# Performance work log

Measured on AMD Instinct MI355X. Metric: run time of the kernel, lower is better.

The kernel has to match this reference:

```python
import jax, jax.numpy as jnp
import numpy as np

TEMPERATURE = 0.07
TIME_THRESH = 5.0 * 1e6  # microseconds


def setup_inputs() -> dict:
    key = jax.random.key(0)
    k1, k2, k3 = jax.random.split(key, 3)
    B, D = 8192, 512
    desc = jax.random.normal(k1, (B, D), dtype=jnp.float32)
    desc = desc / jnp.linalg.norm(desc, axis=-1, keepdims=True)  # module expects normalized descriptors
    seq_ids = jax.random.randint(k2, (B,), 0, 64, dtype=jnp.int64)
    time_mid = jax.random.randint(k3, (B,), 0, 20_000_000, dtype=jnp.int64)
    return {"descriptors": desc, "seq_ids": seq_ids, "time_mid": time_mid}


def reference(descriptors, seq_ids, time_mid):
    B = descriptors.shape[0]
    # [B, B] temperature-scaled cosine similarities
    logits = jnp.matmul(descriptors, descriptors.T) / TEMPERATURE

    eye = jnp.eye(B, dtype=bool)
    same_seq = seq_ids[:, None] == seq_ids[None, :]
    close_time = jnp.abs(time_mid[:, None] - time_mid[None, :]).astype(jnp.float32) < TIME_THRESH
    pos_mask = same_seq & close_time & ~eye  # positives
    offdiag = ~eye                            # positives + negatives = denominator support

    # denominator per row i: log sum_{j != i} exp(logits[i, j])
    denom_lse = jax.nn.logsumexp(jnp.where(offdiag, logits, -jnp.inf), axis=1)  # [B]

    # per positive pair (i, j): -log( exp(l_ij) / denom_i ) = denom_lse_i - l_ij
    pair_loss = jnp.where(pos_mask, denom_lse[:, None] - logits, 0.0)
    num_pos = jnp.sum(pos_mask)
    loss = jnp.sum(pair_loss) / jnp.maximum(num_pos, 1).astype(pair_loss.dtype)
    return loss
```

## Files before the change

kernel.cpp:

```cpp
#include <hip/hip_runtime.h>
#include <math.h>

#define TILE 128

typedef __attribute__((ext_vector_type(4))) float f32x4;
typedef __attribute__((ext_vector_type(2))) long long llong2;

#define INV_T    14.285714285714286f
#define K2C      20.60992915f
#define K2C8     0.32203014296875f
#define INV_T64  0.22321428571428573f
#define TIME_THR 5000000

__device__ __forceinline__ unsigned pack_bf16x2(float lo, float hi) {
  unsigned a = __float_as_uint(lo);
  unsigned b = __float_as_uint(hi);
  a = (a + 0x7FFFu + ((a >> 16) & 1u)) >> 16;
  b = (b + 0x7FFFu + ((b >> 16) & 1u)) & 0xFFFF0000u;
  return b | a;
}

__device__ __forceinline__ unsigned f32_to_e4m3(float x) {
  unsigned u = __float_as_uint(x);
  unsigned s = (u >> 24) & 0x80u;
  int e = (int)((u >> 23) & 0xffu) - 127;
  unsigned m = u & 0x7fffffu;
  if (e < -9) return s;
  if (e < -6) {
    int sh = 20 + (-6 - e);
    unsigned full = (1u << 23) | m;
    unsigned q = full >> sh;
    unsigned rem = full & ((1u << sh) - 1u);
    unsigned half = 1u << (sh - 1);
    if (rem > half || (rem == half && (q & 1u))) q++;
    return s | q;
  }
  unsigned q = m >> 20;
  unsigned rem = m & 0xfffffu;
  if (rem > 0x80000u || (rem == 0x80000u && (q & 1u))) q++;
  int ee = e;
  if (q == 8u) { q = 0u; ee++; }
  if (ee > 8 || (ee == 8 && q == 7u)) return s | 0x7eu;
  return s | (unsigned)((ee + 7) << 3) | q;
}

__device__ __forceinline__ void gl_lds16(const void* g, void* l) {
  __builtin_amdgcn_global_load_lds(
      (const __attribute__((address_space(1))) unsigned int*)g,
      (__attribute__((address_space(3))) unsigned int*)l, 16, 0, 0);
}

template <int MODE>
__device__ __forceinline__ void infonce_body(
    const float* __restrict__ desc, const unsigned char* __restrict__ desc8,
    const int* __restrict__ seq, const int* __restrict__ tmid,
    float* __restrict__ p_se, float* __restrict__ p_ps,
    float* __restrict__ p_pc, int B, int D, int NB) {
  const int T = NB * (NB + 1) / 2;
  int t = blockIdx.x;
  if ((T & 7) == 0) t = (t & 7) * (T >> 3) + (t >> 3);
  float fn = (float)NB + 0.5f;
  int r = (int)(fn - sqrtf(fmaxf(fn * fn - 2.0f * (float)t, 0.0f)));
  if (r < 0) r = 0;
  if (r > NB - 1) r = NB - 1;
  auto Sf = [NB](int rr) { return rr * NB - ((rr * (rr - 1)) >> 1); };
  while (r > 0 && Sf(r) > t) --r;
  while (r < NB - 1 && Sf(r + 1) <= t) ++r;
  const int rb = r;
  const int cb = rb + (t - Sf(rb));
  const bool upper = (cb != rb);

  const int row0 = rb * TILE;
  const int col0 = cb * TILE;

  const int tid = threadIdx.x;
  const int l = tid & 63;
  const int w = tid >> 6;
  const int wrow = (w >> 1) << 6;
  const int wcol = (w & 1) << 6;
  const int lr = l & 15;
  const int kg = l >> 4;

  f32x4 acc[4][4];
#pragma unroll
  for (int m = 0; m < 4; ++m)
#pragma unroll
    for (int n = 0; n < 4; ++n) acc[m][n] = (f32x4){0.f, 0.f, 0.f, 0.f};

  const int sr = tid >> 3;
  const int sc = tid & 7;

  if (MODE == 2) {
    __shared__ __align__(16) unsigned char lA8[2][TILE][128];
    __shared__ __align__(16) unsigned char lB8[TILE][128];
    __shared__ int mseq_r[TILE], mtim_r[TILE], mseq_c[TILE], mtim_c[TILE];

    if (tid < TILE) {
      mseq_r[tid] = seq[row0 + tid];
      mtim_r[tid] = tmid[row0 + tid];
      mseq_c[tid] = seq[col0 + tid];
      mtim_c[tid] = tmid[col0 + tid];
    }

    const int NT = D >> 7;
    const unsigned char* pa =
        desc8 + (size_t)(row0 + (tid >> 3)) * D + (tid & 7) * 16;
    const unsigned char* pb =
        desc8 + (size_t)(col0 + (tid >> 3)) * D + (tid & 7) * 16;
    const size_t rstep = (size_t)32 * D;

    auto stageA = [&](int bu_, int tt) {
      const int off = tt << 7;
#pragma unroll
      for (int q = 0; q < 4; ++q)
        gl_lds16(pa + (size_t)q * rstep + off,
                 (char*)&lA8[bu_][0][0] + (q << 12) + tid * 16);
    };
    auto stageB = [&](int tt) {
      const int off = tt << 7;
#pragma unroll
      for (int q = 0; q < 4; ++q)
        gl_lds16(pb + (size_t)q * rstep + off,
                 (char*)&lB8[0][0] + (q << 12) + tid * 16);
    };

    __builtin_amdgcn_sched_barrier(0);
    stageA(0, 0);
    stageB(0);
    __builtin_amdgcn_sched_barrier(0);

    for (int ts = 0; ts < NT; ++ts) {
      const int bu = ts & 1;
      if (ts + 1 < NT) {
        stageA(bu ^ 1, ts + 1);
        __builtin_amdgcn_sched_barrier(0);
        asm volatile("s_waitcnt vmcnt(4)" ::: "memory");
      } else {
        asm volatile("s_waitcnt vmcnt(0)" ::: "memory");
      }
      __builtin_amdgcn_sched_barrier(0);
      __builtin_amdgcn_s_barrier();
      __builtin_amdgcn_sched_barrier(0);

      llong2 av[4][2], bv[4][2];
#pragma unroll
      for (int m = 0; m < 4; ++m) {
        const int row = wrow + (m << 4) + lr;
#pragma unroll
        for (int j2 = 0; j2 < 2; ++j2) {
          const int ch = ((j2 << 2) + kg) ^ (row & 7);
          av[m][j2] =
              *reinterpret_cast<const llong2*>(&lA8[bu][row][ch << 4]);
        }
      }
#pragma unroll
      for (int n = 0; n < 4; ++n) {
        const int row = wcol + (n << 4) + lr;
#pragma unroll
        for (int j2 = 0; j2 < 2; ++j2) {
          const int ch = ((j2 << 2) + kg) ^ (row & 7);
          bv[n][j2] = *reinterpret_cast<const llong2*>(&lB8[row][ch << 4]);
        }
      }
      __builtin_amdgcn_sched_barrier(0);
      asm volatile("s_waitcnt lgkmcnt(0)" ::: "memory");
      __builtin_amdgcn_sched_barrier(0);
      __builtin_amdgcn_s_setprio(1);
#pragma unroll
      for (int j2 = 0; j2 < 2; ++j2)
#pragma unroll
        for (int kk = 0; kk < 2; ++kk)
#pragma unroll
          for (int m = 0; m < 4; ++m)
#pragma unroll
            for (int n = 0; n < 4; ++n)
              acc[m][n] = __builtin_amdgcn_mfma_f32_16x16x32_fp8_fp8(
                  av[m][j2][kk], bv[n][j2][kk], acc[m][n], 0, 0, 0);
      __builtin_amdgcn_s_setprio(0);
      __builtin_amdgcn_sched_barrier(0);
      __builtin_amdgcn_s_barrier();
      __builtin_amdgcn_sched_barrier(0);
      if (ts + 1 < NT) stageB(ts + 1);
      __builtin_amdgcn_sched_barrier(0);
    }
    __syncthreads();

    float* rowred = (float*)&lA8[0][0][0];
    float* colred = (float*)&lB8[0][0];

    int cseq[4], ctim[4], gcol[4];
#pragma unroll
    for (int n = 0; n < 4; ++n) {
      const int cl = wcol + (n << 4) + lr;
      cseq[n] = mseq_c[cl];
      ctim[n] = mtim_c[cl];
      gcol[n] = col0 + cl;
    }
    float colse[4] = {0.f, 0.f, 0.f, 0.f};
    float colpd[4] = {0.f, 0.f, 0.f, 0.f};
    float colpc[4] = {0.f, 0.f, 0.f, 0.f};

#pragma unroll
    for (int m = 0; m < 4; ++m) {
#pragma unroll
      for (int reg = 0; reg < 4; ++reg) {
        const int rl = wrow + (m << 4) + (kg << 2) + reg;
        const int growg = row0 + rl;
        const int rs = mseq_r[rl];
        const int rt = mtim_r[rl];
        float se = 0.f, pd = 0.f, pcnt = 0.f;
#pragma unroll
        for (int n = 0; n < 4; ++n) {
          const float dot = acc[m][n][reg];
          const float e = exp2f(fmaf(dot, K2C8, -K2C));
          const bool nd = (growg != gcol[n]);
          int dt = rt - ctim[n];
          dt = dt < 0 ? -dt : dt;
          const bool pos = nd && (rs == cseq[n]) && (dt < TIME_THR);
          const float ev = nd ? e : 0.f;
          const float dv = pos ? dot : 0.f;
          const float cv = pos ? 1.f : 0.f;
          se += ev;
          pd += dv;
          pcnt += cv;
          colse[n] += ev;
          colpd[n] += dv;
          colpc[n] += cv;
        }
#pragma unroll
        for (int s = 1; s < 16; s <<= 1) {
          se += __shfl_xor(se, s);
          pd += __shfl_xor(pd, s);
          pcnt += __shfl_xor(pcnt, s);
        }
        if (lr == 0) {
          const int half = wcol >> 6;
          float* rr3 = rowred + ((size_t)(half * TILE + rl)) * 3;
          rr3[0] = se;
          rr3[1] = pd;
          rr3[2] = pcnt;
        }
      }
    }
    if (upper) {
#pragma unroll
      for (int n = 0; n < 4; ++n) {
        float cs = colse[n], cp = colpd[n], cc = colpc[n];
        cs += __shfl_xor(cs, 16);
        cp += __shfl_xor(cp, 16);
        cc += __shfl_xor(cc, 16);
        cs += __shfl_xor(cs, 32);
        cp += __shfl_xor(cp, 32);
        cc += __shfl_xor(cc, 32);
        if (l < 16) {
          const int half = wrow >> 6;
          const int cl = wcol + (n << 4) + lr;
          float* cr3 = colred + ((size_t)(half * TILE + cl)) * 3;
          cr3[0] = cs;
          cr3[1] = cp;
          cr3[2] = cc;
        }
      }
    }
    __syncthreads();

    if (tid < TILE) {
      const int row = tid;
      const float se =
          rowred[(size_t)row * 3 + 0] + rowred[(size_t)(TILE + row) * 3 + 0];
      const float pd =
          rowred[(size_t)row * 3 + 1] + rowred[(size_t)(TILE + row) * 3 + 1];
      const float pc =
          rowred[(size_t)row * 3 + 2] + rowred[(size_t)(TILE + row) * 3 + 2];
      const size_t o = (size_t)cb * B + row0 + row;
      p_se[o] = se;
      p_ps[o] = pd * INV_T64;
      p_pc[o] = pc;
    } else if (upper && tid < 2 * TILE) {
      const int col = tid - TILE;
      const float se =
          colred[(size_t)col * 3 + 0] + colred[(size_t)(TILE + col) * 3 + 0];
      const float pd =
          colred[(size_t)col * 3 + 1] + colred[(size_t)(TILE + col) * 3 + 1];
      const float pc =
          colred[(size_t)col * 3 + 2] + colred[(size_t)(TILE + col) * 3 + 2];
      const size_t o = (size_t)rb * B + col0 + col;
      p_se[o] = se;
      p_ps[o] = pd * INV_T64;
      p_pc[o] = pc;
    }
  } else {
    __shared__ __align__(16) unsigned short lAw[TILE][64];
    __shared__ __align__(16) unsigned short lBw[TILE][64];
    __shared__ int mseq_r[TILE], mtim_r[TILE], mseq_c[TILE], mtim_c[TILE];
    typedef __attribute__((ext_vector_type(8))) short short8v;

    if (tid < TILE) {
      mseq_r[tid] = seq[row0 + tid];
      mtim_r[tid] = tmid[row0 + tid];
      mseq_c[tid] = seq[col0 + tid];
      mtim_c[tid] = tmid[col0 + tid];
    }
    for (int k0 = 0; k0 < D; k0 += 64) {
      __syncthreads();
#pragma unroll
      for (int p = 0; p < 4; ++p) {
        const int rr = (p << 5) + sr;
        const float* gA = desc + (size_t)(row0 + rr) * D + k0 + (sc << 3);
        const float4 fa0 = *reinterpret_cast<const float4*>(gA);
        const float4 fa1 = *reinterpret_cast<const float4*>(gA + 4);
        const float* gB = desc + (size_t)(col0 + rr) * D + k0 + (sc << 3);
        const float4 fb0 = *reinterpret_cast<const float4*>(gB);
        const float4 fb1 = *reinterpret_cast<const float4*>(gB + 4);
        uint4 wa, wb;
        wa.x = pack_bf16x2(fa0.x, fa0.y);
        wa.y = pack_bf16x2(fa0.z, fa0.w);
        wa.z = pack_bf16x2(fa1.x, fa1.y);
        wa.w = pack_bf16x2(fa1.z, fa1.w);
        wb.x = pack_bf16x2(fb0.x, fb0.y);
        wb.y = pack_bf16x2(fb0.z, fb0.w);
        wb.z = pack_bf16x2(fb1.x, fb1.y);
        wb.w = pack_bf16x2(fb1.z, fb1.w);
        const int dst = (sc ^ (rr & 7)) << 3;
        *reinterpret_cast<uint4*>(&lAw[rr][dst]) = wa;
        *reinterpret_cast<uint4*>(&lBw[rr][dst]) = wb;
      }
      __syncthreads();
#pragma unroll
      for (int kk = 0; kk < 2; ++kk) {
        short8v af[4], bf[4];
#pragma unroll
        for (int m = 0; m < 4; ++m) {
          const int rowa = wrow + (m << 4) + lr;
          const int ch = ((kk << 2) + kg) ^ (rowa & 7);
          af[m] = *reinterpret_cast<const short8v*>(&lAw[rowa][ch << 3]);
        }
#pragma unroll
        for (int n = 0; n < 4; ++n) {
          const int rowb = wcol + (n << 4) + lr;
          const int ch = ((kk << 2) + kg) ^ (rowb & 7);
          bf[n] = *reinterpret_cast<const short8v*>(&lBw[rowb][ch << 3]);
        }
#pragma unroll
        for (int m = 0; m < 4; ++m)
#pragma unroll
          for (int n = 0; n < 4; ++n)
            acc[m][n] = __builtin_amdgcn_mfma_f32_16x16x32_bf16(af[m], bf[n],
                                                                acc[m][n], 0, 0, 0);
      }
    }
    __syncthreads();

    int cseq[4], ctim[4], gcol[4];
#pragma unroll
    for (int n = 0; n < 4; ++n) {
      const int cl = wcol + (n << 4) + lr;
      cseq[n] = mseq_c[cl];
      ctim[n] = mtim_c[cl];
      gcol[n] = col0 + cl;
    }
    float colse[4] = {0.f, 0.f, 0.f, 0.f};
    float colpd[4] = {0.f, 0.f, 0.f, 0.f};
    float colpc[4] = {0.f, 0.f, 0.f, 0.f};

#pragma unroll
    for (int m = 0; m < 4; ++m) {
#pragma unroll
      for (int reg = 0; reg < 4; ++reg) {
        const int rl = wrow + (m << 4) + (kg << 2) + reg;
        const int growg = row0 + rl;
        const int rs = mseq_r[rl];
        const int rt = mtim_r[rl];
        float se = 0.f, pd = 0.f, pcnt = 0.f;
#pragma unroll
        for (int n = 0; n < 4; ++n) {
          const float dot = acc[m][n][reg];
          const float e = exp2f(fmaf(dot, K2C, -K2C));
          const bool nd = (growg != gcol[n]);
          int dt = rt - ctim[n];
          dt = dt < 0 ? -dt : dt;
          const bool pos = nd && (rs == cseq[n]) && (dt < TIME_THR);
          const float ev = nd ? e : 0.f;
          const float dv = pos ? dot : 0.f;
          const float cv = pos ? 1.f : 0.f;
          se += ev;
          pd += dv;
          pcnt += cv;
          if (upper) {
            colse[n] += ev;
            colpd[n] += dv;
            colpc[n] += cv;
          }
        }
#pragma unroll
        for (int s = 1; s < 16; s <<= 1) {
          se += __shfl_xor(se, s);
          pd += __shfl_xor(pd, s);
          pcnt += __shfl_xor(pcnt, s);
        }
        if ((l & 15) == 0) {
          atomicAdd(&p_se[growg], se);
          atomicAdd(&p_ps[growg], pd * INV_T);
          atomicAdd(&p_pc[growg], pcnt);
        }
      }
    }
    if (upper) {
#pragma unroll
      for (int n = 0; n < 4; ++n) {
        float cs = colse[n], cp = colpd[n], cc = colpc[n];
        cs += __shfl_xor(cs, 16);
        cp += __shfl_xor(cp, 16);
        cc += __shfl_xor(cc, 16);
        cs += __shfl_xor(cs, 32);
        cp += __shfl_xor(cp, 32);
        cc += __shfl_xor(cc, 32);
        if (kg == 0) {
          atomicAdd(&p_se[gcol[n]], cs);
          atomicAdd(&p_ps[gcol[n]], cp * INV_T);
          atomicAdd(&p_pc[gcol[n]], cc);
        }
      }
    }
  }
}

__global__ __launch_bounds__(256, 3) void infonce_main2(
    const float* desc, const unsigned char* desc8, const int* seq,
    const int* tmid, float* p_se, float* p_ps, float* p_pc, int B, int D,
    int NB) {
  infonce_body<2>(desc, desc8, seq, tmid, p_se, p_ps, p_pc, B, D, NB);
}
__global__ __launch_bounds__(256, 2) void infonce_main0(
    const float* desc, const unsigned char* desc8, const int* seq,
    const int* tmid, float* p_se, float* p_ps, float* p_pc, int B, int D,
    int NB) {
  infonce_body<0>(desc, desc8, seq, tmid, p_se, p_ps, p_pc, B, D, NB);
}

__global__ __launch_bounds__(256) void conv_fp8(const float* __restrict__ in,
                                                unsigned char* __restrict__ out,
                                                int D, int nchunk) {
  const int u = blockIdx.x * 256 + threadIdx.x;
  if (u >= nchunk) return;
  const int cpr = D >> 4;
  const int r = u / cpr;
  const int cc = u - r * cpr;
  const int kt = cc >> 3;
  const int p = cc & 7;
  const int g = p ^ (r & 7);
  const int j2 = g >> 2;
  const int kgc = g & 3;
  const float* src = in + (size_t)r * D + (kt << 7) + (j2 << 6) + (kgc << 3);
  const float4 f0 = *reinterpret_cast<const float4*>(src);
  const float4 f1 = *reinterpret_cast<const float4*>(src + 4);
  const float4 g0 = *reinterpret_cast<const float4*>(src + 32);
  const float4 g1 = *reinterpret_cast<const float4*>(src + 36);
  unsigned char b[16];
  b[0] = f32_to_e4m3(f0.x * 8.f);
  b[1] = f32_to_e4m3(f0.y * 8.f);
  b[2] = f32_to_e4m3(f0.z * 8.f);
  b[3] = f32_to_e4m3(f0.w * 8.f);
  b[4] = f32_to_e4m3(f1.x * 8.f);
  b[5] = f32_to_e4m3(f1.y * 8.f);
  b[6] = f32_to_e4m3(f1.z * 8.f);
  b[7] = f32_to_e4m3(f1.w * 8.f);
  b[8] = f32_to_e4m3(g0.x * 8.f);
  b[9] = f32_to_e4m3(g0.y * 8.f);
  b[10] = f32_to_e4m3(g0.z * 8.f);
  b[11] = f32_to_e4m3(g0.w * 8.f);
  b[12] = f32_to_e4m3(g1.x * 8.f);
  b[13] = f32_to_e4m3(g1.y * 8.f);
  b[14] = f32_to_e4m3(g1.z * 8.f);
  b[15] = f32_to_e4m3(g1.w * 8.f);
  uint4 wv;
  unsigned* wp = (unsigned*)&wv;
#pragma unroll
  for (int d = 0; d < 4; ++d)
    wp[d] = (unsigned)b[d * 4] | ((unsigned)b[d * 4 + 1] << 8) |
            ((unsigned)b[d * 4 + 2] << 16) | ((unsigned)b[d * 4 + 3] << 24);
  *reinterpret_cast<uint4*>(out + (size_t)u * 16) = wv;
}

__global__ __launch_bounds__(256) void reduce_parts4(
    const float* __restrict__ p_se, const float* __restrict__ p_ps,
    const float* __restrict__ p_pc, float* __restrict__ bnum,
    float* __restrict__ bcnt, int B, int NB) {
  const int tid = threadIdx.x;
  const int rloc = tid & 63;
  const int chunk = tid >> 6;
  const int row = blockIdx.x * 64 + rloc;
  const int jpc = NB >> 2;
  float se = 0.f, ps = 0.f, pc = 0.f;
  for (int j = chunk * jpc; j < (chunk + 1) * jpc; ++j) {
    const size_t o = (size_t)j * B + row;
    se += p_se[o];
    ps += p_ps[o];
    pc += p_pc[o];
  }
  __shared__ float s3[3][4][64];
  s3[0][chunk][rloc] = se;
  s3[1][chunk][rloc] = ps;
  s3[2][chunk][rloc] = pc;
  __syncthreads();
  if (tid < 64) {
    const float tse = s3[0][0][tid] + s3[0][1][tid] + s3[0][2][tid] + s3[0][3][tid];
    const float tps = s3[1][0][tid] + s3[1][1][tid] + s3[1][2][tid] + s3[1][3][tid];
    const float tpc = s3[2][0][tid] + s3[2][1][tid] + s3[2][2][tid] + s3[2][3][tid];
    float a = tpc * (logf(tse) + INV_T) - tps;
    float b = tpc;
#pragma unroll
    for (int s = 1; s < 64; s <<= 1) {
      a += __shfl_xor(a, s);
      b += __shfl_xor(b, s);
    }
    if (tid == 0) {
      bnum[blockIdx.x] = a;
      bcnt[blockIdx.x] = b;
    }
  }
}

__global__ __launch_bounds__(256) void final_reduce(
    const float* __restrict__ bnum, const float* __restrict__ bcnt,
    float* __restrict__ out, int n) {
  __shared__ float sn[256];
  __shared__ float sc[256];
  const int tid = threadIdx.x;
  float a = 0.f, b = 0.f;
  for (int i = tid; i < n; i += 256) {
    a += bnum[i];
    b += bcnt[i];
  }
  sn[tid] = a;
  sc[tid] = b;
  __syncthreads();
  for (int s = 128; s > 0; s >>= 1) {
    if (tid < s) {
      sn[tid] += sn[tid + s];
      sc[tid] += sc[tid + s];
    }
    __syncthreads();
  }
  if (tid == 0) out[0] = sn[0] / fmaxf(sc[0], 1.f);
}

__global__ __launch_bounds__(1024) void infonce_finalize(
    const float* __restrict__ a_se, const float* __restrict__ a_ps,
    const float* __restrict__ a_pc, float* __restrict__ out, int B) {
  __shared__ float sn[1024];
  __shared__ float sc[1024];
  const int tid = threadIdx.x;
  float num = 0.f, cnt = 0.f;
  for (int i = tid; i < B; i += 1024) {
    const float c = a_pc[i];
    num += c * (logf(a_se[i]) + INV_T) - a_ps[i];
    cnt += c;
  }
  sn[tid] = num;
  sc[tid] = cnt;
  __syncthreads();
  for (int s = 512; s > 0; s >>= 1) {
    if (tid < s) {
      sn[tid] += sn[tid + s];
      sc[tid] += sc[tid + s];
    }
    __syncthreads();
  }
  if (tid == 0) out[0] = sn[0] / fmaxf(sc[0], 1.f);
}

extern "C" void kernel_launch(void* const* d_in, const int* in_sizes, int n_in,
                              void* d_out, int out_size, void* d_ws, size_t ws_size,
                              hipStream_t stream) {
  (void)n_in;
  (void)out_size;
  const float* desc = (const float*)d_in[0];
  const int* seq = (const int*)d_in[1];
  const int* tmid = (const int*)d_in[2];
  const int B = in_sizes[1];
  const int D = in_sizes[0] / B;
  const int NB = B / TILE;
  const int T = NB * (NB + 1) / 2;

  const size_t desc8_bytes = (size_t)B * D;
  const size_t parts_elems = (size_t)B * NB;
  const size_t nb1 = (size_t)B / 64;
  const size_t need8 = desc8_bytes + 3 * parts_elems * 4 + 2 * nb1 * 4;

  if ((B & 255) == 0 && (D & 127) == 0 && ws_size >= need8) {
    unsigned char* desc8 = (unsigned char*)d_ws;
    float* p_se = (float*)((char*)d_ws + desc8_bytes);
    float* p_ps = p_se + parts_elems;
    float* p_pc = p_ps + parts_elems;
    float* bnum = p_pc + parts_elems;
    float* bcnt = bnum + nb1;
    const int nchunk = (int)(((size_t)B * D) >> 4);
    conv_fp8<<<(nchunk + 255) / 256, 256, 0, stream>>>(desc, desc8, D, nchunk);
    infonce_main2<<<T, 256, 0, stream>>>(desc, desc8, seq, tmid, p_se, p_ps,
                                         p_pc, B, D, NB);
    const int nrb = B / 64;
    reduce_parts4<<<nrb, 256, 0, stream>>>(p_se, p_ps, p_pc, bnum, bcnt, B, NB);
    final_reduce<<<1, 256, 0, stream>>>(bnum, bcnt, (float*)d_out, nrb);
  } else {
    float* a_se = (float*)d_ws;
    float* a_ps = a_se + B;
    float* a_pc = a_ps + B;
    hipMemsetAsync(d_ws, 0, (size_t)3 * B * sizeof(float), stream);
    infonce_main0<<<T, 256, 0, stream>>>(desc, nullptr, seq, tmid, a_se, a_ps,
                                         a_pc, B, D, NB);
    infonce_finalize<<<1, 1024, 0, stream>>>(a_se, a_ps, a_pc, (float*)d_out, B);
  }
}
```

Measured before the change: 109.7 us.

## Make FP8 tile kernel persistent and prefetch next tile across tile boundaries

Replaces the one-block-per-tile FP8 similarity kernel with a persistent kernel of up to 512 blocks that loop over triangular tiles. The first K-slice of the next tile is prefetched during the last K-step of the current one, so global-to-LDS loads overlap the epilogue. B is now double-buffered like A, and seq/time metadata is read from global memory instead of being staged in LDS. The larger LDS footprint at two blocks per CU lowers occupancy compared with the earlier three-blocks-per-CU launch bound, and the epilogue now issues global loads.

```diff
diff --git a/kernel.cpp b/kernel.cpp
--- a/kernel.cpp
+++ b/kernel.cpp
@@ -50,29 +50,17 @@
       (__attribute__((address_space(3))) unsigned int*)l, 16, 0, 0);
 }
 
-template <int MODE>
-__device__ __forceinline__ void infonce_body(
-    const float* __restrict__ desc, const unsigned char* __restrict__ desc8,
-    const int* __restrict__ seq, const int* __restrict__ tmid,
-    float* __restrict__ p_se, float* __restrict__ p_ps,
-    float* __restrict__ p_pc, int B, int D, int NB) {
+__global__ __launch_bounds__(256, 2) void infonce_pers(
+    const unsigned char* __restrict__ desc8, const int* __restrict__ seq,
+    const int* __restrict__ tmid, float* __restrict__ p_se,
+    float* __restrict__ p_ps, float* __restrict__ p_pc, int B, int D, int NB,
+    int G) {
+  __shared__ __align__(16) unsigned char lA8[2][TILE][128];
+  __shared__ __align__(16) unsigned char lB8[2][TILE][128];
+  __shared__ float redR[2 * TILE * 3];
+  __shared__ float redC[2 * TILE * 3];
+
   const int T = NB * (NB + 1) / 2;
-  int t = blockIdx.x;
-  if ((T & 7) == 0) t = (t & 7) * (T >> 3) + (t >> 3);
-  float fn = (float)NB + 0.5f;
-  int r = (int)(fn - sqrtf(fmaxf(fn * fn - 2.0f * (float)t, 0.0f)));
-  if (r < 0) r = 0;
-  if (r > NB - 1) r = NB - 1;
-  auto Sf = [NB](int rr) { return rr * NB - ((rr * (rr - 1)) >> 1); };
-  while (r > 0 && Sf(r) > t) --r;
-  while (r < NB - 1 && Sf(r + 1) <= t) ++r;
-  const int rb = r;
-  const int cb = rb + (t - Sf(rb));
-  const bool upper = (cb != rb);
-
-  const int row0 = rb * TILE;
-  const int col0 = cb * TILE;
-
   const int tid = threadIdx.x;
   const int l = tid & 63;
   const int w = tid >> 6;
@@ -80,6 +68,34 @@
   const int wcol = (w & 1) << 6;
   const int lr = l & 15;
   const int kg = l >> 4;
+  const int NT = D >> 7;
+
+  auto decode = [&](int idx, int& rb_, int& cb_) {
+    int t = idx;
+    if ((T & 7) == 0) t = (t & 7) * (T >> 3) + (t >> 3);
+    float fn = (float)NB + 0.5f;
+    int r = (int)(fn - sqrtf(fmaxf(fn * fn - 2.0f * (float)t, 0.0f)));
+    if (r < 0) r = 0;
+    if (r > NB - 1) r = NB - 1;
+    auto Sf = [&](int rr) { return rr * NB - ((rr * (rr - 1)) >> 1); };
+    while (r > 0 && Sf(r) > t) --r;
+    while (r < NB - 1 && Sf(r + 1) <= t) ++r;
+    rb_ = r;
+    cb_ = r + (t - Sf(r));
+  };
+
+  const size_t rstep = (size_t)32 * D;
+  const size_t lane_off = (size_t)(tid >> 3) * D + (size_t)(tid & 7) * 16;
+  auto stage = [&](const unsigned char* src, unsigned char* dst) {
+#pragma unroll
+    for (int q = 0; q < 4; ++q)
+      gl_lds16(src + (size_t)q * rstep, dst + (q << 12) + tid * 16);
+  };
+
+  int rb, cb;
+  decode(blockIdx.x, rb, cb);
+  const unsigned char* paCur = desc8 + (size_t)(rb * TILE) * D + lane_off;
+  const unsigned char* pbCur = desc8 + (size_t)(cb * TILE) * D + lane_off;
 
   f32x4 acc[4][4];
 #pragma unroll
@@ -87,54 +103,37 @@
 #pragma unroll
     for (int n = 0; n < 4; ++n) acc[m][n] = (f32x4){0.f, 0.f, 0.f, 0.f};
 
-  const int sr = tid >> 3;
-  const int sc = tid & 7;
-
-  if (MODE == 2) {
-    __shared__ __align__(16) unsigned char lA8[2][TILE][128];
-    __shared__ __align__(16) unsigned char lB8[TILE][128];
-    __shared__ int mseq_r[TILE], mtim_r[TILE], mseq_c[TILE], mtim_c[TILE];
-
-    if (tid < TILE) {
-      mseq_r[tid] = seq[row0 + tid];
-      mtim_r[tid] = tmid[row0 + tid];
-      mseq_c[tid] = seq[col0 + tid];
-      mtim_c[tid] = tmid[col0 + tid];
-    }
-
-    const int NT = D >> 7;
-    const unsigned char* pa =
-        desc8 + (size_t)(row0 + (tid >> 3)) * D + (tid & 7) * 16;
-    const unsigned char* pb =
-        desc8 + (size_t)(col0 + (tid >> 3)) * D + (tid & 7) * 16;
-    const size_t rstep = (size_t)32 * D;
-
-    auto stageA = [&](int bu_, int tt) {
-      const int off = tt << 7;
-#pragma unroll
-      for (int q = 0; q < 4; ++q)
-        gl_lds16(pa + (size_t)q * rstep + off,
-                 (char*)&lA8[bu_][0][0] + (q << 12) + tid * 16);
-    };
-    auto stageB = [&](int tt) {
-      const int off = tt << 7;
-#pragma unroll
-      for (int q = 0; q < 4; ++q)
-        gl_lds16(pb + (size_t)q * rstep + off,
-                 (char*)&lB8[0][0] + (q << 12) + tid * 16);
-    };
-
-    __builtin_amdgcn_sched_barrier(0);
-    stageA(0, 0);
-    stageB(0);
-    __builtin_amdgcn_sched_barrier(0);
+  __builtin_amdgcn_sched_barrier(0);
+  stage(paCur, &lA8[0][0][0]);
+  stage(pbCur, &lB8[0][0][0]);
+  __builtin_amdgcn_sched_barrier(0);
+
+  int gs = 0;
+  for (int j = blockIdx.x; j < T; j += G) {
+    const int row0 = rb * TILE;
+    const int col0 = cb * TILE;
+    const bool upper = (cb != rb);
+    const bool hasNext = (j + G < T);
+    int nrb = 0, ncb = 0;
+    const unsigned char *paNext = nullptr, *pbNext = nullptr;
+    if (hasNext) {
+      decode(j + G, nrb, ncb);
+      paNext = desc8 + (size_t)(nrb * TILE) * D + lane_off;
+      pbNext = desc8 + (size_t)(ncb * TILE) * D + lane_off;
+    }
 
     for (int ts = 0; ts < NT; ++ts) {
-      const int bu = ts & 1;
+      const int bu = gs & 1;
       if (ts + 1 < NT) {
-        stageA(bu ^ 1, ts + 1);
+        stage(paCur + ((ts + 1) << 7), &lA8[bu ^ 1][0][0]);
+        stage(pbCur + ((ts + 1) << 7), &lB8[bu ^ 1][0][0]);
         __builtin_amdgcn_sched_barrier(0);
-        asm volatile("s_waitcnt vmcnt(4)" ::: "memory");
+        asm volatile("s_waitcnt vmcnt(8)" ::: "memory");
+      } else if (hasNext) {
+        stage(paNext, &lA8[bu ^ 1][0][0]);
+        stage(pbNext, &lB8[bu ^ 1][0][0]);
+        __builtin_amdgcn_sched_barrier(0);
+        asm volatile("s_waitcnt vmcnt(8)" ::: "memory");
       } else {
         asm volatile("s_waitcnt vmcnt(0)" ::: "memory");
       }
@@ -159,7 +158,8 @@
 #pragma unroll
         for (int j2 = 0; j2 < 2; ++j2) {
           const int ch = ((j2 << 2) + kg) ^ (row & 7);
-          bv[n][j2] = *reinterpret_cast<const llong2*>(&lB8[row][ch << 4]);
+          bv[n][j2] =
+              *reinterpret_cast<const llong2*>(&lB8[bu][row][ch << 4]);
         }
       }
       __builtin_amdgcn_sched_barrier(0);
@@ -179,22 +179,16 @@
       __builtin_amdgcn_s_setprio(0);
       __builtin_amdgcn_sched_barrier(0);
       __builtin_amdgcn_s_barrier();
-      __builtin_amdgcn_sched_barrier(0);
-      if (ts + 1 < NT) stageB(ts + 1);
-      __builtin_amdgcn_sched_barrier(0);
-    }
-    __syncthreads();
-
-    float* rowred = (float*)&lA8[0][0][0];
-    float* colred = (float*)&lB8[0][0];
+      ++gs;
+    }
 
     int cseq[4], ctim[4], gcol[4];
 #pragma unroll
     for (int n = 0; n < 4; ++n) {
       const int cl = wcol + (n << 4) + lr;
-      cseq[n] = mseq_c[cl];
-      ctim[n] = mtim_c[cl];
       gcol[n] = col0 + cl;
+      cseq[n] = seq[gcol[n]];
+      ctim[n] = tmid[gcol[n]];
     }
     float colse[4] = {0.f, 0.f, 0.f, 0.f};
     float colpd[4] = {0.f, 0.f, 0.f, 0.f};
@@ -206,8 +200,8 @@
       for (int reg = 0; reg < 4; ++reg) {
         const int rl = wrow + (m << 4) + (kg << 2) + reg;
         const int growg = row0 + rl;
-        const int rs = mseq_r[rl];
-        const int rt = mtim_r[rl];
+        const int rs = seq[growg];
+        const int rt = tmid[growg];
         float se = 0.f, pd = 0.f, pcnt = 0.f;
 #pragma unroll
         for (int n = 0; n < 4; ++n) {
@@ -235,7 +229,7 @@
         }
         if (lr == 0) {
           const int half = wcol >> 6;
-          float* rr3 = rowred + ((size_t)(half * TILE + rl)) * 3;
+          float* rr3 = redR + ((size_t)(half * TILE + rl)) * 3;
           rr3[0] = se;
           rr3[1] = pd;
           rr3[2] = pcnt;
@@ -255,187 +249,224 @@
         if (l < 16) {
           const int half = wrow >> 6;
           const int cl = wcol + (n << 4) + lr;
-          float* cr3 = colred + ((size_t)(half * TILE + cl)) * 3;
+          float* cr3 = redC + ((size_t)(half * TILE + cl)) * 3;
           cr3[0] = cs;
           cr3[1] = cp;
           cr3[2] = cc;
         }
       }
     }
-    __syncthreads();
+    asm volatile("s_waitcnt lgkmcnt(0)" ::: "memory");
+    __builtin_amdgcn_sched_barrier(0);
+    __builtin_amdgcn_s_barrier();
+    __builtin_amdgcn_sched_barrier(0);
 
     if (tid < TILE) {
       const int row = tid;
       const float se =
-          rowred[(size_t)row * 3 + 0] + rowred[(size_t)(TILE + row) * 3 + 0];
+          redR[(size_t)row * 3 + 0] + redR[(size_t)(TILE + row) * 3 + 0];
       const float pd =
-          rowred[(size_t)row * 3 + 1] + rowred[(size_t)(TILE + row) * 3 + 1];
+          redR[(size_t)row * 3 + 1] + redR[(size_t)(TILE + row) * 3 + 1];
       const float pc =
-          rowred[(size_t)row * 3 + 2] + rowred[(size_t)(TILE + row) * 3 + 2];
+          redR[(size_t)row * 3 + 2] + redR[(size_t)(TILE + row) * 3 + 2];
       const size_t o = (size_t)cb * B + row0 + row;
       p_se[o] = se;
       p_ps[o] = pd * INV_T64;
       p_pc[o] = pc;
-    } else if (upper && tid < 2 * TILE) {
+    } else if (upper) {
       const int col = tid - TILE;
       const float se =
-          colred[(size_t)col * 3 + 0] + colred[(size_t)(TILE + col) * 3 + 0];
+          redC[(size_t)col * 3 + 0] + redC[(size_t)(TILE + col) * 3 + 0];
       const float pd =
-          colred[(size_t)col * 3 + 1] + colred[(size_t)(TILE + col) * 3 + 1];
+          redC[(size_t)col * 3 + 1] + redC[(size_t)(TILE + col) * 3 + 1];
       const float pc =
-          colred[(size_t)col * 3 + 2] + colred[(size_t)(TILE + col) * 3 + 2];
+          redC[(size_t)col * 3 + 2] + redC[(size_t)(TILE + col) * 3 + 2];
       const size_t o = (size_t)rb * B + col0 + col;
       p_se[o] = se;
       p_ps[o] = pd * INV_T64;
       p_pc[o] = pc;
     }
-  } else {
-    __shared__ __align__(16) unsigned short lAw[TILE][64];
-    __shared__ __align__(16) unsigned short lBw[TILE][64];
-    __shared__ int mseq_r[TILE], mtim_r[TILE], mseq_c[TILE], mtim_c[TILE];
-    typedef __attribute__((ext_vector_type(8))) short short8v;
-
-    if (tid < TILE) {
-      mseq_r[tid] = seq[row0 + tid];
-      mtim_r[tid] = tmid[row0 + tid];
-      mseq_c[tid] = seq[col0 + tid];
-      mtim_c[tid] = tmid[col0 + tid];
-    }
-    for (int k0 = 0; k0 < D; k0 += 64) {
-      __syncthreads();
-#pragma unroll
-      for (int p = 0; p < 4; ++p) {
-        const int rr = (p << 5) + sr;
-        const float* gA = desc + (size_t)(row0 + rr) * D + k0 + (sc << 3);
-        const float4 fa0 = *reinterpret_cast<const float4*>(gA);
-        const float4 fa1 = *reinterpret_cast<const float4*>(gA + 4);
-        const float* gB = desc + (size_t)(col0 + rr) * D + k0 + (sc << 3);
-        const float4 fb0 = *reinterpret_cast<const float4*>(gB);
-        const float4 fb1 = *reinterpret_cast<const float4*>(gB + 4);
-        uint4 wa, wb;
-        wa.x = pack_bf16x2(fa0.x, fa0.y);
-        wa.y = pack_bf16x2(fa0.z, fa0.w);
-        wa.z = pack_bf16x2(fa1.x, fa1.y);
-        wa.w = pack_bf16x2(fa1.z, fa1.w);
-        wb.x = pack_bf16x2(fb0.x, fb0.y);
-        wb.y = pack_bf16x2(fb0.z, fb0.w);
-        wb.z = pack_bf16x2(fb1.x, fb1.y);
-        wb.w = pack_bf16x2(fb1.z, fb1.w);
-        const int dst = (sc ^ (rr & 7)) << 3;
-        *reinterpret_cast<uint4*>(&lAw[rr][dst]) = wa;
-        *reinterpret_cast<uint4*>(&lBw[rr][dst]) = wb;
-      }
-      __syncthreads();
-#pragma unroll
-      for (int kk = 0; kk < 2; ++kk) {
-        short8v af[4], bf[4];
-#pragma unroll
-        for (int m = 0; m < 4; ++m) {
-          const int rowa = wrow + (m << 4) + lr;
-          const int ch = ((kk << 2) + kg) ^ (rowa & 7);
-          af[m] = *reinterpret_cast<const short8v*>(&lAw[rowa][ch << 3]);
+
+    rb = nrb;
+    cb = ncb;
+    paCur = paNext;
+    pbCur = pbNext;
+#pragma unroll
+    for (int m = 0; m < 4; ++m)
+#pragma unroll
+      for (int n = 0; n < 4; ++n) acc[m][n] = (f32x4){0.f, 0.f, 0.f, 0.f};
+  }
+}
+
+__global__ __launch_bounds__(256, 2) void infonce_fb(
+    const float* __restrict__ desc, const int* __restrict__ seq,
+    const int* __restrict__ tmid, float* __restrict__ a_se,
+    float* __restrict__ a_ps, float* __restrict__ a_pc, int B, int D, int NB) {
+  __shared__ __align__(16) unsigned short lAw[TILE][64];
+  __shared__ __align__(16) unsigned short lBw[TILE][64];
+  __shared__ int mseq_r[TILE], mtim_r[TILE], mseq_c[TILE], mtim_c[TILE];
+  typedef __attribute__((ext_vector_type(8))) short short8v;
+
+  const int T = NB * (NB + 1) / 2;
+  int t = blockIdx.x;
+  if ((T & 7) == 0) t = (t & 7) * (T >> 3) + (t >> 3);
+  float fn = (float)NB + 0.5f;
+  int r = (int)(fn - sqrtf(fmaxf(fn * fn - 2.0f * (float)t, 0.0f)));
+  if (r < 0) r = 0;
+  if (r > NB - 1) r = NB - 1;
+  auto Sf = [NB](int rr) { return rr * NB - ((rr * (rr - 1)) >> 1); };
+  while (r > 0 && Sf(r) > t) --r;
+  while (r < NB - 1 && Sf(r + 1) <= t) ++r;
+  const int rb = r;
+  const int cb = rb + (t - Sf(rb));
+  const bool upper = (cb != rb);
+  const int row0 = rb * TILE;
+  const int col0 = cb * TILE;
+
+  const int tid = threadIdx.x;
+  const int l = tid & 63;
+  const int w = tid >> 6;
+  const int wrow = (w >> 1) << 6;
+  const int wcol = (w & 1) << 6;
+  const int lr = l & 15;
+  const int kg = l >> 4;
+  const int sr = tid >> 3;
+  const int sc = tid & 7;
+
+  if (tid < TILE) {
+    mseq_r[tid] = seq[row0 + tid];
+    mtim_r[tid] = tmid[row0 + tid];
+    mseq_c[tid] = seq[col0 + tid];
+    mtim_c[tid] = tmid[col0 + tid];
+  }
+
+  f32x4 acc[4][4];
+#pragma unroll
+  for (int m = 0; m < 4; ++m)
+#pragma unroll
+    for (int n = 0; n < 4; ++n) acc[m][n] = (f32x4){0.f, 0.f, 0.f, 0.f};
+
+  for (int k0 = 0; k0 < D; k0 += 64) {
+    __syncthreads();
+#pragma unroll
+    for (int p = 0; p < 4; ++p) {
+      const int rr = (p << 5) + sr;
+      const float* gA = desc + (size_t)(row0 + rr) * D + k0 + (sc << 3);
+      const float4 fa0 = *reinterpret_cast<const float4*>(gA);
+      const float4 fa1 = *reinterpret_cast<const float4*>(gA + 4);
+      const float* gB = desc + (size_t)(col0 + rr) * D + k0 + (sc << 3);
+      const float4 fb0 = *reinterpret_cast<const float4*>(gB);
+      const float4 fb1 = *reinterpret_cast<const float4*>(gB + 4);
+      uint4 wa, wb;
+      wa.x = pack_bf16x2(fa0.x, fa0.y);
+      wa.y = pack_bf16x2(fa0.z, fa0.w);
+      wa.z = pack_bf16x2(fa1.x, fa1.y);
+      wa.w = pack_bf16x2(fa1.z, fa1.w);
+      wb.x = pack_bf16x2(fb0.x, fb0.y);
+      wb.y = pack_bf16x2(fb0.z, fb0.w);
+      wb.z = pack_bf16x2(fb1.x, fb1.y);
+      wb.w = pack_bf16x2(fb1.z, fb1.w);
+      const int dst = (sc ^ (rr & 7)) << 3;
+      *reinterpret_cast<uint4*>(&lAw[rr][dst]) = wa;
+      *reinterpret_cast<uint4*>(&lBw[rr][dst]) = wb;
+    }
+    __syncthreads();
+#pragma unroll
+    for (int kk = 0; kk < 2; ++kk) {
+      short8v af[4], bf[4];
+#pragma unroll
+      for (int m = 0; m < 4; ++m) {
+        const int rowa = wrow + (m << 4) + lr;
+        const int ch = ((kk << 2) + kg) ^ (rowa & 7);
+        af[m] = *reinterpret_cast<const short8v*>(&lAw[rowa][ch << 3]);
+      }
+#pragma unroll
+      for (int n = 0; n < 4; ++n) {
+        const int rowb = wcol + (n << 4) + lr;
+        const int ch = ((kk << 2) + kg) ^ (rowb & 7);
+        bf[n] = *reinterpret_cast<const short8v*>(&lBw[rowb][ch << 3]);
+      }
+#pragma unroll
+      for (int m = 0; m < 4; ++m)
+#pragma unroll
+        for (int n = 0; n < 4; ++n)
+          acc[m][n] = __builtin_amdgcn_mfma_f32_16x16x32_bf16(af[m], bf[n],
+                                                              acc[m][n], 0, 0, 0);
+    }
+  }
+  __syncthreads();
+
+  int cseq[4], ctim[4], gcol[4];
+#pragma unroll
+  for (int n = 0; n < 4; ++n) {
+    const int cl = wcol + (n << 4) + lr;
+    cseq[n] = mseq_c[cl];
+    ctim[n] = mtim_c[cl];
+    gcol[n] = col0 + cl;
+  }
+  float colse[4] = {0.f, 0.f, 0.f, 0.f};
+  float colpd[4] = {0.f, 0.f, 0.f, 0.f};
+  float colpc[4] = {0.f, 0.f, 0.f, 0.f};
+
+#pragma unroll
+  for (int m = 0; m < 4; ++m) {
+#pragma unroll
+    for (int reg = 0; reg < 4; ++reg) {
+      const int rl = wrow + (m << 4) + (kg << 2) + reg;
+      const int growg = row0 + rl;
+      const int rs = mseq_r[rl];
+      const int rt = mtim_r[rl];
+      float se = 0.f, pd = 0.f, pcnt = 0.f;
+#pragma unroll
+      for (int n = 0; n < 4; ++n) {
+        const float dot = acc[m][n][reg];
+        const float e = exp2f(fmaf(dot, K2C, -K2C));
+        const bool nd = (growg != gcol[n]);
+        int dt = rt - ctim[n];
+        dt = dt < 0 ? -dt : dt;
+        const bool pos = nd && (rs == cseq[n]) && (dt < TIME_THR);
+        const float ev = nd ? e : 0.f;
+        const float dv = pos ? dot : 0.f;
+        const float cv = pos ? 1.f : 0.f;
+        se += ev;
+        pd += dv;
+        pcnt += cv;
+        if (upper) {
+          colse[n] += ev;
+          colpd[n] += dv;
+          colpc[n] += cv;
         }
-#pragma unroll
-        for (int n = 0; n < 4; ++n) {
-          const int rowb = wcol + (n << 4) + lr;
-          const int ch = ((kk << 2) + kg) ^ (rowb & 7);
-          bf[n] = *reinterpret_cast<const short8v*>(&lBw[rowb][ch << 3]);
-        }
-#pragma unroll
-        for (int m = 0; m < 4; ++m)
-#pragma unroll
-          for (int n = 0; n < 4; ++n)
-            acc[m][n] = __builtin_amdgcn_mfma_f32_16x16x32_bf16(af[m], bf[n],
-                                                                acc[m][n], 0, 0, 0);
-      }
-    }
-    __syncthreads();
-
-    int cseq[4], ctim[4], gcol[4];
+      }
+#pragma unroll
+      for (int s = 1; s < 16; s <<= 1) {
+        se += __shfl_xor(se, s);
+        pd += __shfl_xor(pd, s);
+        pcnt += __shfl_xor(pcnt, s);
+      }
+      if ((l & 15) == 0) {
+        atomicAdd(&a_se[growg], se);
+        atomicAdd(&a_ps[growg], pd * INV_T);
+        atomicAdd(&a_pc[growg], pcnt);
+      }
+    }
+  }
+  if (upper) {
 #pragma unroll
     for (int n = 0; n < 4; ++n) {
-      const int cl = wcol + (n << 4) + lr;
-      cseq[n] = mseq_c[cl];
-      ctim[n] = mtim_c[cl];
-      gcol[n] = col0 + cl;
-    }
-    float colse[4] = {0.f, 0.f, 0.f, 0.f};
-    float colpd[4] = {0.f, 0.f, 0.f, 0.f};
-    float colpc[4] = {0.f, 0.f, 0.f, 0.f};
-
-#pragma unroll
-    for (int m = 0; m < 4; ++m) {
-#pragma unroll
-      for (int reg = 0; reg < 4; ++reg) {
-        const int rl = wrow + (m << 4) + (kg << 2) + reg;
-        const int growg = row0 + rl;
-        const int rs = mseq_r[rl];
-        const int rt = mtim_r[rl];
-        float se = 0.f, pd = 0.f, pcnt = 0.f;
-#pragma unroll
-        for (int n = 0; n < 4; ++n) {
-          const float dot = acc[m][n][reg];
-          const float e = exp2f(fmaf(dot, K2C, -K2C));
-          const bool nd = (growg != gcol[n]);
-          int dt = rt - ctim[n];
-          dt = dt < 0 ? -dt : dt;
-          const bool pos = nd && (rs == cseq[n]) && (dt < TIME_THR);
-          const float ev = nd ? e : 0.f;
-          const float dv = pos ? dot : 0.f;
-          const float cv = pos ? 1.f : 0.f;
-          se += ev;
-          pd += dv;
-          pcnt += cv;
-          if (upper) {
-            colse[n] += ev;
-            colpd[n] += dv;
-            colpc[n] += cv;
-          }
-        }
-#pragma unroll
-        for (int s = 1; s < 16; s <<= 1) {
-          se += __shfl_xor(se, s);
-          pd += __shfl_xor(pd, s);
-          pcnt += __shfl_xor(pcnt, s);
-        }
-        if ((l & 15) == 0) {
-          atomicAdd(&p_se[growg], se);
-          atomicAdd(&p_ps[growg], pd * INV_T);
-          atomicAdd(&p_pc[growg], pcnt);
-        }
-      }
-    }
-    if (upper) {
-#pragma unroll
-      for (int n = 0; n < 4; ++n) {
-        float cs = colse[n], cp = colpd[n], cc = colpc[n];
-        cs += __shfl_xor(cs, 16);
-        cp += __shfl_xor(cp, 16);
-        cc += __shfl_xor(cc, 16);
-        cs += __shfl_xor(cs, 32);
-        cp += __shfl_xor(cp, 32);
-        cc += __shfl_xor(cc, 32);
-        if (kg == 0) {
-          atomicAdd(&p_se[gcol[n]], cs);
-          atomicAdd(&p_ps[gcol[n]], cp * INV_T);
-          atomicAdd(&p_pc[gcol[n]], cc);
-        }
-      }
-    }
-  }
-}
-
-__global__ __launch_bounds__(256, 3) void infonce_main2(
-    const float* desc, const unsigned char* desc8, const int* seq,
-    const int* tmid, float* p_se, float* p_ps, float* p_pc, int B, int D,
-    int NB) {
-  infonce_body<2>(desc, desc8, seq, tmid, p_se, p_ps, p_pc, B, D, NB);
-}
-__global__ __launch_bounds__(256, 2) void infonce_main0(
-    const float* desc, const unsigned char* desc8, const int* seq,
-    const int* tmid, float* p_se, float* p_ps, float* p_pc, int B, int D,
-    int NB) {
-  infonce_body<0>(desc, desc8, seq, tmid, p_se, p_ps, p_pc, B, D, NB);
+      float cs = colse[n], cp = colpd[n], cc = colpc[n];
+      cs += __shfl_xor(cs, 16);
+      cp += __shfl_xor(cp, 16);
+      cc += __shfl_xor(cc, 16);
+      cs += __shfl_xor(cs, 32);
+      cp += __shfl_xor(cp, 32);
+      cc += __shfl_xor(cc, 32);
+      if (kg == 0) {
+        atomicAdd(&a_se[gcol[n]], cs);
+        atomicAdd(&a_ps[gcol[n]], cp * INV_T);
+        atomicAdd(&a_pc[gcol[n]], cc);
+      }
+    }
+  }
 }
 
 __global__ __launch_bounds__(256) void conv_fp8(const float* __restrict__ in,
@@ -597,8 +628,9 @@
     float* bcnt = bnum + nb1;
     const int nchunk = (int)(((size_t)B * D) >> 4);
     conv_fp8<<<(nchunk + 255) / 256, 256, 0, stream>>>(desc, desc8, D, nchunk);
-    infonce_main2<<<T, 256, 0, stream>>>(desc, desc8, seq, tmid, p_se, p_ps,
-                                         p_pc, B, D, NB);
+    const int G = T < 512 ? T : 512;
+    infonce_pers<<<G, 256, 0, stream>>>(desc8, seq, tmid, p_se, p_ps, p_pc, B,
+                                        D, NB, G);
     const int nrb = B / 64;
     reduce_parts4<<<nrb, 256, 0, stream>>>(p_se, p_ps, p_pc, bnum, bcnt, B, NB);
     final_reduce<<<1, 256, 0, stream>>>(bnum, bcnt, (float*)d_out, nrb);
@@ -607,8 +639,8 @@
     float* a_ps = a_se + B;
     float* a_pc = a_ps + B;
     hipMemsetAsync(d_ws, 0, (size_t)3 * B * sizeof(float), stream);
-    infonce_main0<<<T, 256, 0, stream>>>(desc, nullptr, seq, tmid, a_se, a_ps,
-                                         a_pc, B, D, NB);
+    infonce_fb<<<T, 256, 0, stream>>>(desc, seq, tmid, a_se, a_ps, a_pc, B, D,
+                                      NB);
     infonce_finalize<<<1, 1024, 0, stream>>>(a_se, a_ps, a_pc, (float*)d_out, B);
   }
 }
```

After: 92.69 us. -15.5%, faster.
